# Optimization experiments

Hardware: AMD Instinct MI355X
Metric: run time of the kernel (lower is better)

Reference implementation:

```python
import jax, jax.numpy as jnp
import numpy as np

N_NODES = 100000
N_EDGES = 3200000
N_FEAT = 128
N_GRAPHS = 256


def setup_inputs() -> dict:
    key = jax.random.key(0)
    ks = jax.random.split(key, 12)
    x = jax.random.normal(ks[0], (N_NODES, N_FEAT), dtype=jnp.float32)
    edge_index = jax.random.randint(ks[1], (2, N_EDGES), 0, N_NODES, dtype=jnp.int64)
    edge_weight = jax.random.uniform(ks[2], (N_EDGES,), dtype=jnp.float32)
    batch = jnp.sort(jax.random.randint(ks[3], (N_NODES,), 0, N_GRAPHS, dtype=jnp.int64))
    def glorot(k, shape):
        lim = np.sqrt(6.0 / (shape[0] + shape[1]))
        return jax.random.uniform(k, shape, dtype=jnp.float32, minval=-lim, maxval=lim)
    W1 = glorot(ks[4], (N_FEAT, 64))
    b1 = jnp.zeros((64,), dtype=jnp.float32)
    W2 = glorot(ks[5], (64, 32))
    b2 = jnp.zeros((32,), dtype=jnp.float32)
    Wl1 = glorot(ks[6], (32, 16))
    bl1 = jnp.zeros((16,), dtype=jnp.float32)
    Wl2 = glorot(ks[7], (16, 1))
    bl2 = jnp.zeros((1,), dtype=jnp.float32)
    return {"x": x, "edge_index": edge_index, "edge_weight": edge_weight,
            "batch": batch, "W1": W1, "b1": b1, "W2": W2, "b2": b2,
            "Wl1": Wl1, "bl1": bl1, "Wl2": Wl2, "bl2": bl2}


def gcn_conv(x, row, col, ew, W, b, num_nodes):
    # x' = D^-1/2 (A + I) D^-1/2 (x W) + b, weights on edges, self-loop weight 1
    h = x @ W  # [N, out]
    deg = jax.ops.segment_sum(ew, col, num_segments=num_nodes) + 1.0  # self-loops add 1
    dinv = jnp.where(deg > 0, jax.lax.rsqrt(deg), 0.0)
    norm = dinv[row] * ew * dinv[col]  # [E]
    msg = h[row] * norm[:, None]  # edge-wise gather + scale
    agg = jax.ops.segment_sum(msg, col, num_segments=num_nodes)
    agg = agg + h * (dinv * dinv)[:, None]  # self-loop contribution
    return agg + b


def reference(x, edge_index, edge_weight, batch, W1, b1, W2, b2, Wl1, bl1, Wl2, bl2):
    row, col = edge_index[0], edge_index[1]
    h = jax.nn.relu(gcn_conv(x, row, col, edge_weight, W1, b1, N_NODES))
    # dropout is identity in eval mode
    h = gcn_conv(h, row, col, edge_weight, W2, b2, N_NODES)
    u = jax.ops.segment_sum(h, batch, num_segments=N_GRAPHS)  # global_add_pool
    out = jax.nn.relu(u @ Wl1 + bl1)
    out = out @ Wl2 + bl2
    return out.reshape(-1)
```

## Files before the change

### kernel.cpp

```cpp
#include <hip/hip_runtime.h>
#include <hip/hip_bf16.h>

#define N_NODES 100000
#define N_EDGES 3200000
#define N_GRAPHS 256

#define NBUCK 391
#define SORT_ITEMS 2048
#define NB_SORT ((N_EDGES + SORT_ITEMS - 1) / SORT_ITEMS)
#define HIST_N (NBUCK * NB_SORT)
#define ROW_MASK 131071

__device__ __forceinline__ float bf2f(unsigned short u) {
    return __uint_as_float(((unsigned)u) << 16);
}
__device__ __forceinline__ unsigned short f2bf(float f) {
    __hip_bfloat16 b = __float2bfloat16(f);
    return *(unsigned short*)&b;
}

__global__ __launch_bounds__(256) void hist_kernel(const int* __restrict__ col,
                                                   int* __restrict__ hist) {
    __shared__ int h[NBUCK];
    int tid = threadIdx.x;
    for (int i = tid; i < NBUCK; i += 256) h[i] = 0;
    __syncthreads();
    int base = blockIdx.x * SORT_ITEMS + tid * 4;
    #pragma unroll
    for (int l = 0; l < SORT_ITEMS / 1024; ++l) {
        int e = base + l * 1024;
        if (e < N_EDGES) {
            int4 c4 = *(const int4*)&col[e];
            atomicAdd(&h[c4.x >> 8], 1);
            atomicAdd(&h[c4.y >> 8], 1);
            atomicAdd(&h[c4.z >> 8], 1);
            atomicAdd(&h[c4.w >> 8], 1);
        }
    }
    __syncthreads();
    for (int i = tid; i < NBUCK; i += 256) hist[i * NB_SORT + blockIdx.x] = h[i];
}

__global__ __launch_bounds__(256) void scanA_kernel(int* __restrict__ a,
                                                    int* __restrict__ bsum, int n) {
    __shared__ int s[256];
    int tid = threadIdx.x;
    int base = blockIdx.x * 4096 + tid * 16;
    int v[16];
    int sum = 0;
    #pragma unroll
    for (int i = 0; i < 16; ++i) { v[i] = (base + i < n) ? a[base + i] : 0; sum += v[i]; }
    s[tid] = sum;
    __syncthreads();
    for (int d = 1; d < 256; d <<= 1) {
        int x = (tid >= d) ? s[tid - d] : 0;
        __syncthreads();
        s[tid] += x;
        __syncthreads();
    }
    int run = s[tid] - sum;
    #pragma unroll
    for (int i = 0; i < 16; ++i) {
        if (base + i < n) a[base + i] = run;
        run += v[i];
    }
    if (tid == 255) bsum[blockIdx.x] = s[255];
}

__global__ __launch_bounds__(256) void scanB_kernel(int* bsum, int nb) {
    __shared__ int s[256];
    int tid = threadIdx.x;
    int v = (tid < nb) ? bsum[tid] : 0;
    s[tid] = v;
    __syncthreads();
    for (int d = 1; d < 256; d <<= 1) {
        int x = (tid >= d) ? s[tid - d] : 0;
        __syncthreads();
        s[tid] += x;
        __syncthreads();
    }
    if (tid < nb) bsum[tid] = s[tid] - v;
}

__global__ __launch_bounds__(256) void scanC_kernel(int* a, const int* __restrict__ bsum, int n) {
    int i = blockIdx.x * 256 + threadIdx.x;
    if (i < n) a[i] += bsum[i >> 12];
}

__global__ __launch_bounds__(256) void scatter_sort_kernel(const int* __restrict__ col,
                                                           const int* __restrict__ row,
                                                           const float* __restrict__ ew,
                                                           const int* __restrict__ hist,
                                                           int2* __restrict__ rw2) {
    __shared__ int offs[NBUCK];
    int tid = threadIdx.x;
    for (int i = tid; i < NBUCK; i += 256) offs[i] = hist[i * NB_SORT + blockIdx.x];
    __syncthreads();
    int base = blockIdx.x * SORT_ITEMS + tid * 4;
    #pragma unroll
    for (int l = 0; l < SORT_ITEMS / 1024; ++l) {
        int e = base + l * 1024;
        if (e < N_EDGES) {
            int4 c4 = *(const int4*)&col[e];
            int4 r4 = *(const int4*)&row[e];
            float4 w4 = *(const float4*)&ew[e];
            int p0 = atomicAdd(&offs[c4.x >> 8], 1);
            int p1 = atomicAdd(&offs[c4.y >> 8], 1);
            int p2 = atomicAdd(&offs[c4.z >> 8], 1);
            int p3 = atomicAdd(&offs[c4.w >> 8], 1);
            int2 v0; v0.x = r4.x | ((c4.x & 255) << 17); v0.y = __float_as_int(w4.x);
            int2 v1; v1.x = r4.y | ((c4.y & 255) << 17); v1.y = __float_as_int(w4.y);
            int2 v2; v2.x = r4.z | ((c4.z & 255) << 17); v2.y = __float_as_int(w4.z);
            int2 v3; v3.x = r4.w | ((c4.w & 255) << 17); v3.y = __float_as_int(w4.w);
            rw2[p0] = v0;
            rw2[p1] = v1;
            rw2[p2] = v2;
            rw2[p3] = v3;
        }
    }
}

__global__ __launch_bounds__(256) void build_kernel(const int* __restrict__ hist,
                                                    const int2* __restrict__ rw2,
                                                    int* __restrict__ off,
                                                    int* __restrict__ cnt,
                                                    float* __restrict__ dinv,
                                                    int2* __restrict__ csr) {
    int b = blockIdx.x;
    int tid = threadIdx.x;
    int begin = hist[b * NB_SORT];
    int end = (b + 1 < NBUCK) ? hist[(b + 1) * NB_SORT] : N_EDGES;
    __shared__ int lcnt[256];
    __shared__ float ldeg[256];
    __shared__ int s[256];
    __shared__ int curo[256];
    lcnt[tid] = 0;
    ldeg[tid] = 0.f;
    __syncthreads();
    for (int e = begin + tid; e < end; e += 512) {
        int2 a = rw2[e];
        int e2 = e + 256;
        int2 c = (e2 < end) ? rw2[e2] : make_int2(0, 0);
        atomicAdd(&lcnt[a.x >> 17], 1);
        atomicAdd(&ldeg[a.x >> 17], __int_as_float(a.y));
        if (e2 < end) {
            atomicAdd(&lcnt[c.x >> 17], 1);
            atomicAdd(&ldeg[c.x >> 17], __int_as_float(c.y));
        }
    }
    __syncthreads();
    int v = lcnt[tid];
    s[tid] = v;
    __syncthreads();
    for (int d = 1; d < 256; d <<= 1) {
        int x = (tid >= d) ? s[tid - d] : 0;
        __syncthreads();
        s[tid] += x;
        __syncthreads();
    }
    int excl = s[tid] - v;
    int node = (b << 8) + tid;
    if (node < N_NODES) {
        off[node] = begin + excl;
        cnt[node] = v;
        dinv[node] = rsqrtf(1.0f + ldeg[tid]);
    }
    curo[tid] = begin + excl;
    __syncthreads();
    for (int e = begin + tid; e < end; e += 512) {
        int2 a = rw2[e];
        int e2 = e + 256;
        int2 c = (e2 < end) ? rw2[e2] : make_int2(0, 0);
        int pa = atomicAdd(&curo[a.x >> 17], 1);
        csr[pa] = make_int2(a.x & ROW_MASK, a.y);
        if (e2 < end) {
            int pc = atomicAdd(&curo[c.x >> 17], 1);
            csr[pc] = make_int2(c.x & ROW_MASK, c.y);
        }
    }
}

template <int IN, int OUT, int ROWS>
__global__ __launch_bounds__(256) void gemm_bf16_kernel(const float* __restrict__ X,
                                                        const float* __restrict__ W,
                                                        const float* __restrict__ scale,
                                                        unsigned short* __restrict__ H, int n) {
    constexpr int BK = 16;
    constexpr int TX = OUT / 4;
    constexpr int TY = ROWS / 4;
    static_assert(TX * TY == 256, "block must be 256 threads");
    constexpr int XSS = ROWS + 4;
    constexpr int WSS = OUT + 4;
    __shared__ float xsT[BK][XSS];
    __shared__ float ws[BK][WSS];
    int tid = threadIdx.x;
    int tx = tid % TX, ty = tid / TX;
    int r0 = blockIdx.x * ROWS;
    float acc[4][4] = {};
    for (int k0 = 0; k0 < IN; k0 += BK) {
        constexpr int XL = (ROWS * BK) / (256 * 4);
        #pragma unroll
        for (int l = 0; l < XL; ++l) {
            int t = tid + l * 256;
            int rr = t >> 2;
            int kp = (t & 3) * 4;
            float4 v = make_float4(0.f, 0.f, 0.f, 0.f);
            int gr = r0 + rr;
            if (gr < n) v = *(const float4*)&X[(size_t)gr * IN + k0 + kp];
            xsT[kp + 0][rr] = v.x;
            xsT[kp + 1][rr] = v.y;
            xsT[kp + 2][rr] = v.z;
            xsT[kp + 3][rr] = v.w;
        }
        constexpr int WL = (BK * OUT) / 4;
        if (tid < WL) {
            int kr = tid / TX;
            int cp = (tid % TX) * 4;
            float4 v = *(const float4*)&W[(size_t)(k0 + kr) * OUT + cp];
            *(float4*)&ws[kr][cp] = v;
        }
        __syncthreads();
        #pragma unroll
        for (int kk = 0; kk < BK; ++kk) {
            float4 a = *(const float4*)&xsT[kk][ty * 4];
            float4 b = *(const float4*)&ws[kk][tx * 4];
            float av[4] = {a.x, a.y, a.z, a.w};
            float bv[4] = {b.x, b.y, b.z, b.w};
            #pragma unroll
            for (int i = 0; i < 4; ++i) {
                #pragma unroll
                for (int j = 0; j < 4; ++j) acc[i][j] = fmaf(av[i], bv[j], acc[i][j]);
            }
        }
        __syncthreads();
    }
    #pragma unroll
    for (int i = 0; i < 4; ++i) {
        int gr = r0 + ty * 4 + i;
        if (gr < n) {
            float sc = scale[gr];
            ushort4 o;
            o.x = f2bf(acc[i][0] * sc);
            o.y = f2bf(acc[i][1] * sc);
            o.z = f2bf(acc[i][2] * sc);
            o.w = f2bf(acc[i][3] * sc);
            *(ushort4*)&H[(size_t)gr * OUT + tx * 4] = o;
        }
    }
}

__global__ __launch_bounds__(256) void agg1_kernel(const int2* __restrict__ csr,
                                                   const int* __restrict__ off,
                                                   const int* __restrict__ cnt,
                                                   const float* __restrict__ dinv,
                                                   const unsigned short* __restrict__ h1t,
                                                   const float* __restrict__ b1,
                                                   float* __restrict__ h1p) {
    int lane = threadIdx.x & 63;
    int node = blockIdx.x * 4 + (threadIdx.x >> 6);
    int s = off[node], c = cnt[node];
    float acc = 0.f;
    for (int j0 = 0; j0 < c; j0 += 64) {
        int m = min(64, c - j0);
        int2 e = make_int2(0, 0);
        if (lane < m) e = csr[s + j0 + lane];
        int jj = 0;
        for (; jj + 8 <= m; jj += 8) {
            int r[8], w[8];
            #pragma unroll
            for (int i = 0; i < 8; ++i) {
                r[i] = __builtin_amdgcn_readlane(e.x, jj + i);
                w[i] = __builtin_amdgcn_readlane(e.y, jj + i);
            }
            unsigned short g[8];
            #pragma unroll
            for (int i = 0; i < 8; ++i) g[i] = h1t[(size_t)r[i] * 64 + lane];
            #pragma unroll
            for (int i = 0; i < 8; ++i) acc = fmaf(__int_as_float(w[i]), bf2f(g[i]), acc);
        }
        for (; jj < m; ++jj) {
            int r = __builtin_amdgcn_readlane(e.x, jj);
            float w = __int_as_float(__builtin_amdgcn_readlane(e.y, jj));
            acc = fmaf(w, bf2f(h1t[(size_t)r * 64 + lane]), acc);
        }
    }
    float di = dinv[node];
    float v = (acc + bf2f(h1t[(size_t)node * 64 + lane])) * di + b1[lane];
    h1p[(size_t)node * 64 + lane] = fmaxf(v, 0.f);
}

__global__ __launch_bounds__(256) void agg2_kernel(const int2* __restrict__ csr,
                                                   const int* __restrict__ off,
                                                   const int* __restrict__ cnt,
                                                   const float* __restrict__ dinv,
                                                   const unsigned short* __restrict__ h2t,
                                                   const float* __restrict__ b2,
                                                   float* __restrict__ h2p) {
    int f = threadIdx.x & 31;
    int half = (threadIdx.x >> 5) & 1;
    int wid = threadIdx.x >> 6;
    int node = blockIdx.x * 8 + wid * 2 + half;
    int s = off[node], c = cnt[node];
    int base = half * 32;
    float acc = 0.f;
    for (int j0 = 0; j0 < c; j0 += 32) {
        int m = min(32, c - j0);
        int2 e = make_int2(0, 0);
        if (f < m) e = csr[s + j0 + f];
        int jj = 0;
        for (; jj + 4 <= m; jj += 4) {
            int r[4], w[4];
            #pragma unroll
            for (int i = 0; i < 4; ++i) {
                r[i] = __shfl(e.x, base + jj + i);
                w[i] = __shfl(e.y, base + jj + i);
            }
            unsigned short g[4];
            #pragma unroll
            for (int i = 0; i < 4; ++i) g[i] = h2t[(size_t)r[i] * 32 + f];
            #pragma unroll
            for (int i = 0; i < 4; ++i) acc = fmaf(__int_as_float(w[i]), bf2f(g[i]), acc);
        }
        for (; jj < m; ++jj) {
            int r = __shfl(e.x, base + jj);
            float w = __int_as_float(__shfl(e.y, base + jj));
            acc = fmaf(w, bf2f(h2t[(size_t)r * 32 + f]), acc);
        }
    }
    float di = dinv[node];
    float v = (acc + bf2f(h2t[(size_t)node * 32 + f])) * di + b2[f];
    h2p[(size_t)node * 32 + f] = v;
}

__global__ __launch_bounds__(256) void pool_kernel(const float* __restrict__ h2p,
                                                   const int* __restrict__ batch,
                                                   float* __restrict__ u) {
    int g = blockIdx.x;
    int lo = 0, hi = N_NODES;
    while (lo < hi) { int m = (lo + hi) >> 1; if (batch[m] < g) lo = m + 1; else hi = m; }
    int start = lo;
    hi = N_NODES;
    while (lo < hi) { int m = (lo + hi) >> 1; if (batch[m] < g + 1) lo = m + 1; else hi = m; }
    int end = lo;
    int f = threadIdx.x & 31, grp = threadIdx.x >> 5;
    float acc = 0.f;
    for (int n = start + grp; n < end; n += 8) acc += h2p[(size_t)n * 32 + f];
    __shared__ float red[8][32];
    red[grp][f] = acc;
    __syncthreads();
    if (threadIdx.x < 32) {
        float sum = 0.f;
        #pragma unroll
        for (int k = 0; k < 8; ++k) sum += red[k][threadIdx.x];
        u[g * 32 + threadIdx.x] = sum;
    }
}

__global__ __launch_bounds__(256) void head_kernel(const float* __restrict__ u,
                                                   const float* __restrict__ Wl1,
                                                   const float* __restrict__ bl1,
                                                   const float* __restrict__ Wl2,
                                                   const float* __restrict__ bl2,
                                                   float* __restrict__ out) {
    int g = threadIdx.x;
    float uu[32];
    #pragma unroll
    for (int k = 0; k < 32; ++k) uu[k] = u[g * 32 + k];
    float o = bl2[0];
    #pragma unroll
    for (int j = 0; j < 16; ++j) {
        float h = bl1[j];
        #pragma unroll
        for (int k = 0; k < 32; ++k) h = fmaf(uu[k], Wl1[k * 16 + j], h);
        o = fmaf(fmaxf(h, 0.f), Wl2[j], o);
    }
    out[g] = o;
}

extern "C" void kernel_launch(void* const* d_in, const int* in_sizes, int n_in,
                              void* d_out, int out_size, void* d_ws, size_t ws_size,
                              hipStream_t stream) {
    const float* x     = (const float*)d_in[0];
    const int*   ei    = (const int*)d_in[1];
    const float* ew    = (const float*)d_in[2];
    const int*   batch = (const int*)d_in[3];
    const float* W1    = (const float*)d_in[4];
    const float* b1    = (const float*)d_in[5];
    const float* W2    = (const float*)d_in[6];
    const float* b2    = (const float*)d_in[7];
    const float* Wl1   = (const float*)d_in[8];
    const float* bl1   = (const float*)d_in[9];
    const float* Wl2   = (const float*)d_in[10];
    const float* bl2   = (const float*)d_in[11];
    float* out = (float*)d_out;

    const int* row = ei;
    const int* col = ei + N_EDGES;

    char* p = (char*)d_ws;
    auto alloc = [&](size_t bytes) {
        char* q = p;
        p += (bytes + 255) & ~(size_t)255;
        return q;
    };
    int*   hist   = (int*)alloc((size_t)HIST_N * 4);
    int*   bsum   = (int*)alloc(1024 * 4);
    int2*  rw2    = (int2*)alloc((size_t)N_EDGES * 8);
    int*   off    = (int*)alloc(N_NODES * 4);
    int*   cnt    = (int*)alloc(N_NODES * 4);
    float* dinv   = (float*)alloc(N_NODES * 4);
    int2*  csr    = (int2*)alloc((size_t)N_EDGES * 8);
    unsigned short* h1t = (unsigned short*)rw2;
    float* h1p    = (float*)alloc((size_t)N_NODES * 64 * 4);
    unsigned short* h2t = (unsigned short*)alloc((size_t)N_NODES * 32 * 2);
    float* h2p    = (float*)alloc((size_t)N_NODES * 32 * 4);
    float* u      = (float*)alloc(N_GRAPHS * 32 * 4);

    const int nbScan = (HIST_N + 4095) / 4096;

    hist_kernel<<<NB_SORT, 256, 0, stream>>>(col, hist);
    scanA_kernel<<<nbScan, 256, 0, stream>>>(hist, bsum, HIST_N);
    scanB_kernel<<<1, 256, 0, stream>>>(bsum, nbScan);
    scanC_kernel<<<(HIST_N + 255) / 256, 256, 0, stream>>>(hist, bsum, HIST_N);
    scatter_sort_kernel<<<NB_SORT, 256, 0, stream>>>(col, row, ew, hist, rw2);
    build_kernel<<<NBUCK, 256, 0, stream>>>(hist, rw2, off, cnt, dinv, csr);

    gemm_bf16_kernel<128, 64, 64><<<(N_NODES + 63) / 64, 256, 0, stream>>>(x, W1, dinv, h1t, N_NODES);
    agg1_kernel<<<(N_NODES + 3) / 4, 256, 0, stream>>>(csr, off, cnt, dinv, h1t, b1, h1p);
    gemm_bf16_kernel<64, 32, 128><<<(N_NODES + 127) / 128, 256, 0, stream>>>(h1p, W2, dinv, h2t, N_NODES);
    agg2_kernel<<<(N_NODES + 7) / 8, 256, 0, stream>>>(csr, off, cnt, dinv, h2t, b2, h2p);
    pool_kernel<<<N_GRAPHS, 256, 0, stream>>>(h2p, batch, u);
    head_kernel<<<1, 256, 0, stream>>>(u, Wl1, bl1, Wl2, bl2, out);
}
```

Measured before the change: 285.3 us.

## Vectorize edge gathers in aggregation kernels with 16-byte loads across edge subgroups

Both aggregation kernels now process several edges at once per wavefront. Each lane loads 8 bf16 features through one 16-byte load instead of one 2-byte scalar load per edge, and partial sums are combined with a shuffle-xor reduction at the end. The aim is to cut the number of memory instructions and raise bytes per gather request in the edge-bound phase. The cost is eight accumulators per lane, a final cross-lane reduction, and padded edge slots with weight zero when the edge count is not a multiple of 8.

```diff
diff --git a/kernel.cpp b/kernel.cpp
--- a/kernel.cpp
+++ b/kernel.cpp
@@ -11,8 +11,11 @@
 #define HIST_N (NBUCK * NB_SORT)
 #define ROW_MASK 131071
 
-__device__ __forceinline__ float bf2f(unsigned short u) {
-    return __uint_as_float(((unsigned)u) << 16);
+__device__ __forceinline__ float bfl(int d) {
+    return __uint_as_float(((unsigned)d) << 16);
+}
+__device__ __forceinline__ float bfh(int d) {
+    return __uint_as_float(((unsigned)d) & 0xffff0000u);
 }
 __device__ __forceinline__ unsigned short f2bf(float f) {
     __hip_bfloat16 b = __float2bfloat16(f);
@@ -258,35 +261,80 @@
                                                    float* __restrict__ h1p) {
     int lane = threadIdx.x & 63;
     int node = blockIdx.x * 4 + (threadIdx.x >> 6);
+    int es = lane >> 3;
+    int fb = lane & 7;
     int s = off[node], c = cnt[node];
-    float acc = 0.f;
+    float acc[8] = {};
     for (int j0 = 0; j0 < c; j0 += 64) {
         int m = min(64, c - j0);
         int2 e = make_int2(0, 0);
         if (lane < m) e = csr[s + j0 + lane];
-        int jj = 0;
-        for (; jj + 8 <= m; jj += 8) {
-            int r[8], w[8];
-            #pragma unroll
-            for (int i = 0; i < 8; ++i) {
-                r[i] = __builtin_amdgcn_readlane(e.x, jj + i);
-                w[i] = __builtin_amdgcn_readlane(e.y, jj + i);
-            }
-            unsigned short g[8];
-            #pragma unroll
-            for (int i = 0; i < 8; ++i) g[i] = h1t[(size_t)r[i] * 64 + lane];
-            #pragma unroll
-            for (int i = 0; i < 8; ++i) acc = fmaf(__int_as_float(w[i]), bf2f(g[i]), acc);
-        }
-        for (; jj < m; ++jj) {
-            int r = __builtin_amdgcn_readlane(e.x, jj);
-            float w = __int_as_float(__builtin_amdgcn_readlane(e.y, jj));
-            acc = fmaf(w, bf2f(h1t[(size_t)r * 64 + lane]), acc);
-        }
-    }
-    float di = dinv[node];
-    float v = (acc + bf2f(h1t[(size_t)node * 64 + lane])) * di + b1[lane];
-    h1p[(size_t)node * 64 + lane] = fmaxf(v, 0.f);
+        int ng = (m + 7) >> 3;
+        int g = 0;
+        for (; g + 2 <= ng; g += 2) {
+            int s0 = g * 8 + es;
+            int s1 = s0 + 8;
+            int r0 = __shfl(e.x, s0);
+            float w0 = __int_as_float(__shfl(e.y, s0));
+            int r1 = __shfl(e.x, s1);
+            float w1 = __int_as_float(__shfl(e.y, s1));
+            int4 d0 = *(const int4*)(h1t + (((size_t)r0) << 6) + (fb << 3));
+            int4 d1 = *(const int4*)(h1t + (((size_t)r1) << 6) + (fb << 3));
+            acc[0] = fmaf(w0, bfl(d0.x), acc[0]);
+            acc[1] = fmaf(w0, bfh(d0.x), acc[1]);
+            acc[2] = fmaf(w0, bfl(d0.y), acc[2]);
+            acc[3] = fmaf(w0, bfh(d0.y), acc[3]);
+            acc[4] = fmaf(w0, bfl(d0.z), acc[4]);
+            acc[5] = fmaf(w0, bfh(d0.z), acc[5]);
+            acc[6] = fmaf(w0, bfl(d0.w), acc[6]);
+            acc[7] = fmaf(w0, bfh(d0.w), acc[7]);
+            acc[0] = fmaf(w1, bfl(d1.x), acc[0]);
+            acc[1] = fmaf(w1, bfh(d1.x), acc[1]);
+            acc[2] = fmaf(w1, bfl(d1.y), acc[2]);
+            acc[3] = fmaf(w1, bfh(d1.y), acc[3]);
+            acc[4] = fmaf(w1, bfl(d1.z), acc[4]);
+            acc[5] = fmaf(w1, bfh(d1.z), acc[5]);
+            acc[6] = fmaf(w1, bfl(d1.w), acc[6]);
+            acc[7] = fmaf(w1, bfh(d1.w), acc[7]);
+        }
+        if (g < ng) {
+            int s0 = g * 8 + es;
+            int r0 = __shfl(e.x, s0);
+            float w0 = __int_as_float(__shfl(e.y, s0));
+            int4 d0 = *(const int4*)(h1t + (((size_t)r0) << 6) + (fb << 3));
+            acc[0] = fmaf(w0, bfl(d0.x), acc[0]);
+            acc[1] = fmaf(w0, bfh(d0.x), acc[1]);
+            acc[2] = fmaf(w0, bfl(d0.y), acc[2]);
+            acc[3] = fmaf(w0, bfh(d0.y), acc[3]);
+            acc[4] = fmaf(w0, bfl(d0.z), acc[4]);
+            acc[5] = fmaf(w0, bfh(d0.z), acc[5]);
+            acc[6] = fmaf(w0, bfl(d0.w), acc[6]);
+            acc[7] = fmaf(w0, bfh(d0.w), acc[7]);
+        }
+    }
+    #pragma unroll
+    for (int mask = 8; mask <= 32; mask <<= 1) {
+        #pragma unroll
+        for (int k = 0; k < 8; ++k) acc[k] += __shfl_xor(acc[k], mask);
+    }
+    if (es == 0) {
+        float di = dinv[node];
+        int4 ds = *(const int4*)(h1t + (((size_t)node) << 6) + (fb << 3));
+        float4 bv0 = *(const float4*)&b1[fb * 8];
+        float4 bv1 = *(const float4*)&b1[fb * 8 + 4];
+        float4 o0, o1;
+        o0.x = fmaxf(fmaf(acc[0] + bfl(ds.x), di, bv0.x), 0.f);
+        o0.y = fmaxf(fmaf(acc[1] + bfh(ds.x), di, bv0.y), 0.f);
+        o0.z = fmaxf(fmaf(acc[2] + bfl(ds.y), di, bv0.z), 0.f);
+        o0.w = fmaxf(fmaf(acc[3] + bfh(ds.y), di, bv0.w), 0.f);
+        o1.x = fmaxf(fmaf(acc[4] + bfl(ds.z), di, bv1.x), 0.f);
+        o1.y = fmaxf(fmaf(acc[5] + bfh(ds.z), di, bv1.y), 0.f);
+        o1.z = fmaxf(fmaf(acc[6] + bfl(ds.w), di, bv1.z), 0.f);
+        o1.w = fmaxf(fmaf(acc[7] + bfh(ds.w), di, bv1.w), 0.f);
+        float* po = h1p + (size_t)node * 64 + fb * 8;
+        *(float4*)po = o0;
+        *(float4*)(po + 4) = o1;
+    }
 }
 
 __global__ __launch_bounds__(256) void agg2_kernel(const int2* __restrict__ csr,
@@ -296,40 +344,86 @@
                                                    const unsigned short* __restrict__ h2t,
                                                    const float* __restrict__ b2,
                                                    float* __restrict__ h2p) {
-    int f = threadIdx.x & 31;
-    int half = (threadIdx.x >> 5) & 1;
+    int lane = threadIdx.x & 63;
+    int half = lane >> 5;
+    int hl = lane & 31;
+    int es = hl >> 2;
+    int fb = hl & 3;
     int wid = threadIdx.x >> 6;
     int node = blockIdx.x * 8 + wid * 2 + half;
     int s = off[node], c = cnt[node];
-    int base = half * 32;
-    float acc = 0.f;
+    int lbase = half << 5;
+    float acc[8] = {};
     for (int j0 = 0; j0 < c; j0 += 32) {
         int m = min(32, c - j0);
         int2 e = make_int2(0, 0);
-        if (f < m) e = csr[s + j0 + f];
-        int jj = 0;
-        for (; jj + 4 <= m; jj += 4) {
-            int r[4], w[4];
-            #pragma unroll
-            for (int i = 0; i < 4; ++i) {
-                r[i] = __shfl(e.x, base + jj + i);
-                w[i] = __shfl(e.y, base + jj + i);
-            }
-            unsigned short g[4];
-            #pragma unroll
-            for (int i = 0; i < 4; ++i) g[i] = h2t[(size_t)r[i] * 32 + f];
-            #pragma unroll
-            for (int i = 0; i < 4; ++i) acc = fmaf(__int_as_float(w[i]), bf2f(g[i]), acc);
-        }
-        for (; jj < m; ++jj) {
-            int r = __shfl(e.x, base + jj);
-            float w = __int_as_float(__shfl(e.y, base + jj));
-            acc = fmaf(w, bf2f(h2t[(size_t)r * 32 + f]), acc);
-        }
-    }
-    float di = dinv[node];
-    float v = (acc + bf2f(h2t[(size_t)node * 32 + f])) * di + b2[f];
-    h2p[(size_t)node * 32 + f] = v;
+        if (hl < m) e = csr[s + j0 + hl];
+        int ng = (m + 7) >> 3;
+        int g = 0;
+        for (; g + 2 <= ng; g += 2) {
+            int s0 = lbase + g * 8 + es;
+            int s1 = s0 + 8;
+            int r0 = __shfl(e.x, s0);
+            float w0 = __int_as_float(__shfl(e.y, s0));
+            int r1 = __shfl(e.x, s1);
+            float w1 = __int_as_float(__shfl(e.y, s1));
+            int4 d0 = *(const int4*)(h2t + (((size_t)r0) << 5) + (fb << 3));
+            int4 d1 = *(const int4*)(h2t + (((size_t)r1) << 5) + (fb << 3));
+            acc[0] = fmaf(w0, bfl(d0.x), acc[0]);
+            acc[1] = fmaf(w0, bfh(d0.x), acc[1]);
+            acc[2] = fmaf(w0, bfl(d0.y), acc[2]);
+            acc[3] = fmaf(w0, bfh(d0.y), acc[3]);
+            acc[4] = fmaf(w0, bfl(d0.z), acc[4]);
+            acc[5] = fmaf(w0, bfh(d0.z), acc[5]);
+            acc[6] = fmaf(w0, bfl(d0.w), acc[6]);
+            acc[7] = fmaf(w0, bfh(d0.w), acc[7]);
+            acc[0] = fmaf(w1, bfl(d1.x), acc[0]);
+            acc[1] = fmaf(w1, bfh(d1.x), acc[1]);
+            acc[2] = fmaf(w1, bfl(d1.y), acc[2]);
+            acc[3] = fmaf(w1, bfh(d1.y), acc[3]);
+            acc[4] = fmaf(w1, bfl(d1.z), acc[4]);
+            acc[5] = fmaf(w1, bfh(d1.z), acc[5]);
+            acc[6] = fmaf(w1, bfl(d1.w), acc[6]);
+            acc[7] = fmaf(w1, bfh(d1.w), acc[7]);
+        }
+        if (g < ng) {
+            int s0 = lbase + g * 8 + es;
+            int r0 = __shfl(e.x, s0);
+            float w0 = __int_as_float(__shfl(e.y, s0));
+            int4 d0 = *(const int4*)(h2t + (((size_t)r0) << 5) + (fb << 3));
+            acc[0] = fmaf(w0, bfl(d0.x), acc[0]);
+            acc[1] = fmaf(w0, bfh(d0.x), acc[1]);
+            acc[2] = fmaf(w0, bfl(d0.y), acc[2]);
+            acc[3] = fmaf(w0, bfh(d0.y), acc[3]);
+            acc[4] = fmaf(w0, bfl(d0.z), acc[4]);
+            acc[5] = fmaf(w0, bfh(d0.z), acc[5]);
+            acc[6] = fmaf(w0, bfl(d0.w), acc[6]);
+            acc[7] = fmaf(w0, bfh(d0.w), acc[7]);
+        }
+    }
+    #pragma unroll
+    for (int mask = 4; mask <= 16; mask <<= 1) {
+        #pragma unroll
+        for (int k = 0; k < 8; ++k) acc[k] += __shfl_xor(acc[k], mask);
+    }
+    if (es == 0) {
+        float di = dinv[node];
+        int4 ds = *(const int4*)(h2t + (((size_t)node) << 5) + (fb << 3));
+        float4 bv0 = *(const float4*)&b2[fb * 8];
+        float4 bv1 = *(const float4*)&b2[fb * 8 + 4];
+        float4 o0, o1;
+        o0.x = fmaf(acc[0] + bfl(ds.x), di, bv0.x);
+        o0.y = fmaf(acc[1] + bfh(ds.x), di, bv0.y);
+        o0.z = fmaf(acc[2] + bfl(ds.y), di, bv0.z);
+        o0.w = fmaf(acc[3] + bfh(ds.y), di, bv0.w);
+        o1.x = fmaf(acc[4] + bfl(ds.z), di, bv1.x);
+        o1.y = fmaf(acc[5] + bfh(ds.z), di, bv1.y);
+        o1.z = fmaf(acc[6] + bfl(ds.w), di, bv1.z);
+        o1.w = fmaf(acc[7] + bfh(ds.w), di, bv1.w);
+        float* po = h2p + (size_t)node * 32 + fb * 8;
+        *(float4*)po = o0;
+        *(float4*)(po + 4) = o1;
+    }
 }
 
 __global__ __launch_bounds__(256) void pool_kernel(const float* __restrict__ h2p,
@@ -426,9 +520,9 @@
     build_kernel<<<NBUCK, 256, 0, stream>>>(hist, rw2, off, cnt, dinv, csr);
 
     gemm_bf16_kernel<128, 64, 64><<<(N_NODES + 63) / 64, 256, 0, stream>>>(x, W1, dinv, h1t, N_NODES);
-    agg1_kernel<<<(N_NODES + 3) / 4, 256, 0, stream>>>(csr, off, cnt, dinv, h1t, b1, h1p);
+    agg1_kernel<<<N_NODES / 4, 256, 0, stream>>>(csr, off, cnt, dinv, h1t, b1, h1p);
     gemm_bf16_kernel<64, 32, 128><<<(N_NODES + 127) / 128, 256, 0, stream>>>(h1p, W2, dinv, h2t, N_NODES);
-    agg2_kernel<<<(N_NODES + 7) / 8, 256, 0, stream>>>(csr, off, cnt, dinv, h2t, b2, h2p);
+    agg2_kernel<<<N_NODES / 8, 256, 0, stream>>>(csr, off, cnt, dinv, h2t, b2, h2p);
     pool_kernel<<<N_GRAPHS, 256, 0, stream>>>(h2p, batch, u);
     head_kernel<<<1, 256, 0, stream>>>(u, Wl1, bl1, Wl2, bl2, out);
 }
```

After: 257.1 us. -9.9%, faster.
